# Performance work log

Measured on AMD Instinct MI355X. Metric: run time of the kernel, lower is better.

The kernel has to match this reference:

```python
import jax, jax.numpy as jnp
import numpy as np

LAYERS, HIDDEN, FFN, HEADS = 4, 128, 256, 4
HEAD_D = HIDDEN // HEADS          # 32
V_HEAD = 2 * HEAD_D               # 64 (double_v_dim)
V_DIM = 2 * HIDDEN                # 256
SCALE_BASE = 512
EPS = 1e-5
GAMMAS = (1.0 - np.exp(np.linspace(np.log(1.0 / 32), np.log(1.0 / 512), HEADS))).astype(np.float32)


def _xpos(x, downscale):
    # x: (..., L, d) -- xpos rotary embedding with per-position decay scale
    L, d = x.shape[-2], x.shape[-1]
    half = d // 2
    base_scale = (jnp.arange(half, dtype=jnp.float32) + 0.4 * d) / (1.4 * d)   # (half,)
    power = jnp.arange(L, dtype=jnp.float32)[:, None] / SCALE_BASE
    sc = base_scale[None, :] ** power                                          # (L, half)
    inv_freq = 1.0 / (10000.0 ** (jnp.arange(half, dtype=jnp.float32) / half))
    ang = jnp.arange(L, dtype=jnp.float32)[:, None] * inv_freq[None, :]        # (L, half)
    sin, cos = jnp.sin(ang), jnp.cos(ang)
    if downscale:
        sc = 1.0 / sc
    sin_d = jnp.repeat(sin * sc, 2, axis=-1)   # duplicate_interleave -> (L, d)
    cos_d = jnp.repeat(cos * sc, 2, axis=-1)
    x1, x2 = x[..., ::2], x[..., 1::2]
    rot = jnp.stack((-x2, x1), axis=-1).reshape(x.shape)  # rotate_every_two
    return x * cos_d + rot * sin_d


def _layer_norm(x, w, b):
    mu = x.mean(-1, keepdims=True)
    var = x.var(-1, keepdims=True)
    return (x - mu) / jnp.sqrt(var + EPS) * w + b


def _msr(X, wq, wk, wv, wg, wo, gn_w, gn_b):
    # MultiScaleRetention, parallel form. X: (B, L, HIDDEN)
    B, L, _ = X.shape
    Q = _xpos(jnp.einsum('blh,nhd->bnld', X, wq), False)   # (B, heads, L, 32)
    K = _xpos(jnp.einsum('blh,nhd->bnld', X, wk), True)
    V = jnp.einsum('blh,nhv->bnlv', X, wv)                 # (B, heads, L, 64)
    n = jnp.arange(L)
    diff = n[:, None] - n[None, :]
    gam = jnp.asarray(GAMMAS)[:, None, None]
    D = jnp.where(diff >= 0, gam ** jnp.maximum(diff, 0).astype(jnp.float32), 0.0)  # (heads, L, L)
    scores = jnp.einsum('bnld,bnmd->bnlm', Q, K) * D[None]
    Y = jnp.einsum('bnlm,bnmv->bnlv', scores, V)
    Y = Y.transpose(0, 2, 1, 3).reshape(B, L, V_DIM)       # concat heads on feature dim
    # GroupNorm(heads, V_DIM) over the channel axis
    Yg = Y.reshape(B, L, HEADS, V_HEAD)
    mu = Yg.mean(-1, keepdims=True)
    var = Yg.var(-1, keepdims=True)
    Yn = ((Yg - mu) / jnp.sqrt(var + EPS)).reshape(B, L, V_DIM) * gn_w + gn_b
    G = X @ wg
    return (G * jax.nn.sigmoid(G) * Yn) @ wo               # swish gate, output proj


def _forward(x, rem_w1, rem_b1, rem_w2, rem_b2, rem_w3, rem_b3,
             wq, wk, wv, wg, wo, gn_w, gn_b,
             ln1_w, ln1_b, ln2_w, ln2_b,
             ffn_w1, ffn_b1, ffn_w2, ffn_b2,
             dec_w1, dec_b1, dec_w2, dec_b2):
    gelu = lambda t: jax.nn.gelu(t, approximate=False)
    # REM: 5 -> 32 -> 64 -> 128, GELU after each linear
    X = gelu(gelu(gelu(x @ rem_w1 + rem_b1) @ rem_w2 + rem_b2) @ rem_w3 + rem_b3)
    # RetNet: pre-LN retention + pre-LN FFN blocks with residuals
    for i in range(LAYERS):
        Y = _msr(_layer_norm(X, ln1_w[i], ln1_b[i]), wq[i], wk[i], wv[i],
                 wg[i], wo[i], gn_w[i], gn_b[i]) + X
        Z = _layer_norm(Y, ln2_w[i], ln2_b[i])
        X = gelu(Z @ ffn_w1[i] + ffn_b1[i]) @ ffn_w2[i] + ffn_b2[i] + Y
    # Decoder: 128 -> 64 -> 20, softmax over classes
    logits = gelu(X @ dec_w1 + dec_b1) @ dec_w2 + dec_b2
    return jax.nn.softmax(logits, axis=-1)


def setup_inputs() -> dict:
    key = jax.random.key(0)
    ks = jax.random.split(key, 16)
    rn = lambda k, shape, s=0.02: jax.random.normal(k, shape, dtype=jnp.float32) * s
    B, L = 64, 512
    return {
        'x': jax.random.normal(ks[0], (B, L, 5), dtype=jnp.float32),
        'rem_w1': rn(ks[1], (5, 32)), 'rem_b1': jnp.zeros((32,), jnp.float32),
        'rem_w2': rn(ks[2], (32, 64)), 'rem_b2': jnp.zeros((64,), jnp.float32),
        'rem_w3': rn(ks[3], (64, HIDDEN)), 'rem_b3': jnp.zeros((HIDDEN,), jnp.float32),
        'wq': rn(ks[4], (LAYERS, HEADS, HIDDEN, HEAD_D), 1.0 / HIDDEN),
        'wk': rn(ks[5], (LAYERS, HEADS, HIDDEN, HEAD_D), 1.0 / HIDDEN),
        'wv': rn(ks[6], (LAYERS, HEADS, HIDDEN, V_HEAD), 1.0 / HIDDEN),
        'wg': rn(ks[7], (LAYERS, HIDDEN, V_DIM), 1.0 / HIDDEN),
        'wo': rn(ks[8], (LAYERS, V_DIM, HIDDEN), 1.0 / HIDDEN),
        'gn_w': jnp.ones((LAYERS, V_DIM), jnp.float32),
        'gn_b': jnp.zeros((LAYERS, V_DIM), jnp.float32),
        'ln1_w': jnp.ones((LAYERS, HIDDEN), jnp.float32),
        'ln1_b': jnp.zeros((LAYERS, HIDDEN), jnp.float32),
        'ln2_w': jnp.ones((LAYERS, HIDDEN), jnp.float32),
        'ln2_b': jnp.zeros((LAYERS, HIDDEN), jnp.float32),
        'ffn_w1': rn(ks[9], (LAYERS, HIDDEN, FFN)),
        'ffn_b1': jnp.zeros((LAYERS, FFN), jnp.float32),
        'ffn_w2': rn(ks[10], (LAYERS, FFN, HIDDEN)),
        'ffn_b2': jnp.zeros((LAYERS, HIDDEN), jnp.float32),
        'dec_w1': rn(ks[11], (HIDDEN, 64)), 'dec_b1': jnp.zeros((64,), jnp.float32),
        'dec_w2': rn(ks[12], (64, 20)), 'dec_b2': jnp.zeros((20,), jnp.float32),
    }


def reference(x, rem_w1, rem_b1, rem_w2, rem_b2, rem_w3, rem_b3,
              wq, wk, wv, wg, wo, gn_w, gn_b,
              ln1_w, ln1_b, ln2_w, ln2_b,
              ffn_w1, ffn_b1, ffn_w2, ffn_b2,
              dec_w1, dec_b1, dec_w2, dec_b2):
    return _forward(x, rem_w1, rem_b1, rem_w2, rem_b2, rem_w3, rem_b3,
                    wq, wk, wv, wg, wo, gn_w, gn_b,
                    ln1_w, ln1_b, ln2_w, ln2_b,
                    ffn_w1, ffn_b1, ffn_w2, ffn_b2,
                    dec_w1, dec_b1, dec_w2, dec_b2)
```

## Files before the change

### kernel.cpp

```cpp
#include <hip/hip_runtime.h>
#include <math.h>
#include <cmath>

#define SEQ   512
#define NBATCH 64
#define BT    32768
#define HID   128
#define NHEAD 4
#define HD    32
#define VHD   64
#define VDIM  256
#define FFND  256

typedef __attribute__((ext_vector_type(8))) short bf16x8;
typedef __attribute__((ext_vector_type(4))) float f32x4;
typedef unsigned short u16;

__device__ __forceinline__ float gelu_f(float x){ return 0.5f*x*(1.f+erff(x*0.70710678118f)); }

__device__ __forceinline__ u16 f2bf(float f){
  union{float f; unsigned u;} v; v.f = f;
  unsigned r = v.u + 0x7FFF + ((v.u>>16)&1);
  return (u16)(r>>16);
}
__device__ __forceinline__ float bf2f(u16 u){
  union{unsigned u; float f;} v; v.u = ((unsigned)u)<<16; return v.f;
}

__device__ __forceinline__ void gload16(const void* g, void* l){
  __builtin_amdgcn_global_load_lds(
      (const __attribute__((address_space(1))) unsigned*)g,
      (__attribute__((address_space(3))) unsigned*)l, 16, 0, 0);
}

#define STAGE_TILE(dst, base, strideU16, colOffU16, wid_, srow_, phys16l_)      \
  do{                                                                           \
    _Pragma("unroll")                                                           \
    for(int it_=0; it_<8; it_++){                                               \
      int blk_ = (wid_)*8 + it_;                                                \
      int row_ = blk_*4 + (srow_);                                              \
      int log16_ = (phys16l_) ^ (row_&15);                                      \
      gload16((base) + (size_t)row_*(strideU16) + (colOffU16) + log16_*8,       \
              &(dst)[blk_*512]);                                                \
    }                                                                           \
  }while(0)

__global__ __launch_bounds__(256) void wconv_kernel(
    const float* __restrict__ wq, const float* __restrict__ wk,
    const float* __restrict__ wv, const float* __restrict__ wg,
    const float* __restrict__ wo, const float* __restrict__ f1,
    const float* __restrict__ f2, const float* __restrict__ dw1,
    const float* __restrict__ w2e, const float* __restrict__ w3e,
    u16* __restrict__ Wt)
{
  int idx = blockIdx.x*256 + threadIdx.x;
  if(idx >= 786432){
    int q = idx - 786432;
    if(q < 8192){ int col=q>>7, h=q&127; Wt[idx]=f2bf(dw1[h*64+col]); }
    else if(q < 10240){ int p=q-8192; int row=p>>5, col=p&31; Wt[idx]=f2bf(w2e[col*64+row]); }
    else { int p=q-10240; int row=p>>6, col=p&63; Wt[idx]=f2bf(w3e[col*128+row]); }
    return;
  }
  int layer = idx / 196608;
  int r = idx - layer*196608;
  u16* W = Wt + (size_t)layer*196608;
  const float* wq_l = wq + (size_t)layer*16384;
  const float* wk_l = wk + (size_t)layer*16384;
  const float* wv_l = wv + (size_t)layer*32768;
  const float* wg_l = wg + (size_t)layer*32768;
  const float* wo_l = wo + (size_t)layer*32768;
  const float* f1_l = f1 + (size_t)layer*32768;
  const float* f2_l = f2 + (size_t)layer*32768;
  float v;
  if(r < 98304){
    int col = r>>7, h = r&127;
    if(col<128){ int n=col>>5, d=col&31; v = wq_l[(n*128+h)*32+d]; }
    else if(col<256){ int c=col-128, n=c>>5, d=c&31; v = wk_l[(n*128+h)*32+d]; }
    else if(col<512){ int c=col-256, n=c>>6, j=c&63; v = wv_l[(n*128+h)*64+j]; }
    else { int p=col-512; v = wg_l[h*256+p]; }
    W[r] = f2bf(v);
  } else if(r < 131072){
    int q = r-98304; int col=q>>8, k=q&255;
    W[r] = f2bf(wo_l[k*128+col]);
  } else if(r < 163840){
    int q = r-131072; int col=q>>7, h=q&127;
    W[r] = f2bf(f1_l[h*256+col]);
  } else {
    int q = r-163840; int col=q>>8, k=q&255;
    W[r] = f2bf(f2_l[k*128+col]);
  }
}

__global__ __launch_bounds__(256) void embed_kernel(
    const float* __restrict__ x,
    const float* __restrict__ w1, const float* __restrict__ b1,
    const float* __restrict__ b2, const float* __restrict__ b3,
    const u16* __restrict__ W23t,
    const float* __restrict__ lnw, const float* __restrict__ lnb,
    float* __restrict__ X, u16* __restrict__ xn)
{
  __shared__ float sx[64][6];
  __shared__ float sw1[160], sb1[32], sb2[64], sb3[128];
  __shared__ u16 big[18944];
  int t=threadIdx.x, lane=t&63, wid=t>>6, mrow=lane&15, quad=lane>>4, r0=wid*16;
  int tok0=blockIdx.x*64;

  for(int i=t;i<320;i+=256) sx[i/5][i%5]=x[(size_t)tok0*5+i];
  for(int i=t;i<160;i+=256) sw1[i]=w1[i];
  if(t<32) sb1[t]=b1[t];
  if(t<64) sb2[t]=b2[t];
  if(t<128) sb3[t]=b3[t];
  for(int c=t;c<256;c+=256){ int row=c>>2, c8=(c&3)*8;
    *(uint4*)&big[2560+row*40+c8]=*(const uint4*)&W23t[row*32+c8]; }
  for(int c=t;c<1024;c+=256){ int row=c>>3, c8=(c&7)*8;
    *(uint4*)&big[9728+row*72+c8]=*(const uint4*)&W23t[2048+row*64+c8]; }
  __syncthreads();

  for(int task=t; task<2048; task+=256){
    int tok=task>>5, j=task&31;
    float a=sb1[j];
    #pragma unroll
    for(int i=0;i<5;i++) a+=sx[tok][i]*sw1[i*32+j];
    big[tok*40+j]=f2bf(gelu_f(a));
  }
  __syncthreads();

  f32x4 h2[4];
  #pragma unroll
  for(int cc=0;cc<4;cc++) h2[cc]=(f32x4){0.f,0.f,0.f,0.f};
  {
    bf16x8 a=*(const bf16x8*)&big[(r0+mrow)*40+quad*8];
    #pragma unroll
    for(int cc=0;cc<4;cc++){
      bf16x8 b=*(const bf16x8*)&big[2560+(cc*16+mrow)*40+quad*8];
      h2[cc]=__builtin_amdgcn_mfma_f32_16x16x32_bf16(a,b,h2[cc],0,0,0);
    }
  }
  #pragma unroll
  for(int cc=0;cc<4;cc++){
    float bs=sb2[cc*16+mrow];
    #pragma unroll
    for(int reg=0;reg<4;reg++)
      big[5120+(r0+quad*4+reg)*72+cc*16+mrow]=f2bf(gelu_f(h2[cc][reg]+bs));
  }
  __syncthreads();

  f32x4 xac[8];
  #pragma unroll
  for(int cc=0;cc<8;cc++) xac[cc]=(f32x4){0.f,0.f,0.f,0.f};
  #pragma unroll
  for(int ks=0;ks<2;ks++){
    bf16x8 a=*(const bf16x8*)&big[5120+(r0+mrow)*72+ks*32+quad*8];
    #pragma unroll
    for(int cc=0;cc<8;cc++){
      bf16x8 b=*(const bf16x8*)&big[9728+(cc*16+mrow)*72+ks*32+quad*8];
      xac[cc]=__builtin_amdgcn_mfma_f32_16x16x32_bf16(a,b,xac[cc],0,0,0);
    }
  }
  __syncthreads();

  #pragma unroll
  for(int reg=0;reg<4;reg++){
    int rowl=r0+quad*4+reg, rowg=tok0+rowl;
    float xv[8], s=0.f, sq=0.f;
    #pragma unroll
    for(int cc=0;cc<8;cc++){
      float v=gelu_f(xac[cc][reg]+sb3[cc*16+mrow]);
      xv[cc]=v; s+=v; sq+=v*v;
    }
    #pragma unroll
    for(int m=1;m<16;m<<=1){ s+=__shfl_xor(s,m); sq+=__shfl_xor(sq,m); }
    float mu=s*(1.f/128.f);
    float var=sq*(1.f/128.f)-mu*mu;
    float rstd=rsqrtf(var+1e-5f);
    #pragma unroll
    for(int cc=0;cc<8;cc++){
      int col=cc*16+mrow;
      X[(size_t)rowg*128+col]=xv[cc];
      big[rowl*136+col]=f2bf((xv[cc]-mu)*rstd*lnw[col]+lnb[col]);
    }
  }
  __syncthreads();
  for(int th=t; th<1024; th+=256){
    int row=th>>4, seg=th&15;
    *(uint4*)&xn[(size_t)(tok0+row)*128+seg*8]=*(const uint4*)&big[row*136+seg*8];
  }
}

__device__ __forceinline__ void qkvg_epilogue(
    int nc, f32x4 acc[2][4], u16* stg,
    int t, int mrow, int quad, int r0q, int c0q, int b, int l0, int tok0,
    u16* __restrict__ Q, u16* __restrict__ K,
    u16* __restrict__ Vt, u16* __restrict__ G)
{
  if(nc < 2){
    bool isK = (nc==1);
    float sgn = isK ? -1.f : 1.f;
    #pragma unroll
    for(int cc=0;cc<4;cc++){
      int colc = c0q + cc*16 + mrow;
      int i = (colc&31)>>1;
      float log2bs = log2f(((float)i + 12.8f)*(1.f/44.8f));
      float invf   = exp2f(-(float)i * (13.28771238f/16.f));
      float rstep  = exp2f(sgn*log2bs*(1.f/512.f));
      float c1 = cosf(invf), s1 = sinf(invf);
      #pragma unroll
      for(int rr=0;rr<2;rr++){
        int rowl0 = r0q + rr*16 + quad*4;
        float lb = (float)(l0 + rowl0);
        float sc = exp2f(sgn*log2bs*lb*(1.f/512.f));
        float ang = lb*invf;
        float u = cosf(ang)*sc, v = sinf(ang)*sc;
        #pragma unroll
        for(int reg=0;reg<4;reg++){
          int rowl = rowl0 + reg;
          float val = acc[rr][cc][reg];
          float partner = __shfl_xor(val, 1);
          float o = (colc&1) ? (val*u + partner*v) : (val*u - partner*v);
          stg[rowl*136 + colc] = f2bf(o);
          float un = (u*c1 - v*s1)*rstep;
          float vn = (u*s1 + v*c1)*rstep;
          u = un; v = vn;
        }
      }
    }
    __syncthreads();
    u16* O = isK ? K : Q;
    for(int th=t; th<1024; th+=256){
      int row=th>>4, n=(th>>2)&3, seg=th&3;
      *(uint4*)&O[(((size_t)(b*4+n)*512) + (l0+row))*32 + seg*8]
        = *(const uint4*)&stg[row*136 + n*32 + seg*8];
    }
  } else if(nc < 4){
    #pragma unroll
    for(int cc=0;cc<4;cc++){
      int colc = c0q + cc*16 + mrow;
      #pragma unroll
      for(int rr=0;rr<2;rr++){
        #pragma unroll
        for(int reg=0;reg<4;reg++){
          int rowl = r0q + rr*16 + quad*4 + reg;
          stg[colc*72 + rowl] = f2bf(acc[rr][cc][reg]);
        }
      }
    }
    __syncthreads();
    int jbase = (nc-2)*128;
    for(int th=t; th<1024; th+=256){
      int row=th>>3, seg=th&7;
      int jg = jbase + row; int n = jg>>6, j = jg&63;
      *(uint4*)&Vt[(((size_t)(b*4+n)*64) + j)*512 + l0 + seg*8]
        = *(const uint4*)&stg[row*72 + seg*8];
    }
  } else {
    #pragma unroll
    for(int cc=0;cc<4;cc++){
      int colc = c0q + cc*16 + mrow;
      #pragma unroll
      for(int rr=0;rr<2;rr++){
        #pragma unroll
        for(int reg=0;reg<4;reg++){
          int rowl = r0q + rr*16 + quad*4 + reg;
          stg[rowl*136 + colc] = f2bf(acc[rr][cc][reg]);
        }
      }
    }
    __syncthreads();
    int gc0 = (nc-4)*128;
    for(int th=t; th<1024; th+=256){
      int row=th>>4, seg=th&15;
      *(uint4*)&G[((size_t)(tok0+row))*256 + gc0 + seg*8]
        = *(const uint4*)&stg[row*136 + seg*8];
    }
  }
}

__global__ __launch_bounds__(256) void qkvg_kernel(
    const u16* __restrict__ A, const u16* __restrict__ Wt,
    u16* __restrict__ Q, u16* __restrict__ K,
    u16* __restrict__ Vt, u16* __restrict__ G)
{
  __shared__ u16 sW[128*128];
  u16* stg = sW;
  int t = threadIdx.x, lane = t&63, wid = t>>6;
  int mrow = lane&15, quad = lane>>4;
  int srow = lane>>4, phys16l = lane&15;
  int r0q = (wid>>1)*32, c0q = (wid&1)*64;
  int tok0 = blockIdx.x*64;
  int b = tok0>>9, l0 = tok0&511;

  bf16x8 a0f[4], a1f[4];
  #pragma unroll
  for(int ks=0; ks<4; ks++){
    a0f[ks] = *(const bf16x8*)&A[(size_t)(tok0+r0q+mrow)*128 + ks*32+quad*8];
    a1f[ks] = *(const bf16x8*)&A[(size_t)(tok0+r0q+16+mrow)*128 + ks*32+quad*8];
  }

  for(int ch=0; ch<3; ch++){
    int nc = blockIdx.y*3 + ch;
    if(ch) __syncthreads();
    STAGE_TILE(sW, Wt + (size_t)nc*16384, 128, 0, wid, srow, phys16l);
    __syncthreads();

    f32x4 acc[2][4];
    #pragma unroll
    for(int rr=0;rr<2;rr++)
      #pragma unroll
      for(int cc=0;cc<4;cc++) acc[rr][cc] = (f32x4){0.f,0.f,0.f,0.f};
    #pragma unroll
    for(int ks=0; ks<4; ks++){
      #pragma unroll
      for(int cc=0; cc<4; cc++){
        bf16x8 bb = *(const bf16x8*)&sW[(c0q+cc*16+mrow)*128 + (((ks*4+quad)^mrow)<<3)];
        acc[0][cc] = __builtin_amdgcn_mfma_f32_16x16x32_bf16(a0f[ks],bb,acc[0][cc],0,0,0);
        acc[1][cc] = __builtin_amdgcn_mfma_f32_16x16x32_bf16(a1f[ks],bb,acc[1][cc],0,0,0);
      }
    }
    __syncthreads();
    qkvg_epilogue(nc, acc, stg, t, mrow, quad, r0q, c0q, b, l0, tok0, Q, K, Vt, G);
  }
}

__global__ __launch_bounds__(256) void mlpq_kernel(
    const u16* __restrict__ Gated, const u16* __restrict__ Wo,
    const u16* __restrict__ W1t, const float* __restrict__ b1,
    const u16* __restrict__ W2t, const float* __restrict__ b2,
    const float* __restrict__ Xin,
    const float* __restrict__ ln2w, const float* __restrict__ ln2b,
    const float* __restrict__ ln1w, const float* __restrict__ ln1b,
    float* __restrict__ Xout,
    const u16* __restrict__ Wq,
    u16* __restrict__ Q, u16* __restrict__ K,
    u16* __restrict__ Vt, u16* __restrict__ G)
{
  __shared__ u16 sW[128*128];
  __shared__ u16 sT[64*136];
  int t=threadIdx.x, lane=t&63, wid=t>>6, mrow=lane&15, quad=lane>>4, r0=wid*16;
  int tok0=blockIdx.x*64;
  int srow = lane>>4, phys16l = lane&15;

  bf16x8 gfrag[8];
  #pragma unroll
  for(int ks=0;ks<8;ks++)
    gfrag[ks]=*(const bf16x8*)&Gated[(size_t)(tok0+r0+mrow)*256 + ks*32+quad*8];

  f32x4 yac[8];
  #pragma unroll
  for(int ch=0;ch<8;ch++) yac[ch]=(f32x4){0.f,0.f,0.f,0.f};
  STAGE_TILE(sW, Wo, 256, 0, wid, srow, phys16l);
  __syncthreads();
  #pragma unroll
  for(int kh=0; kh<2; kh++){
    #pragma unroll
    for(int ch=0;ch<8;ch++){
      #pragma unroll
      for(int ks=0;ks<4;ks++){
        bf16x8 b=*(const bf16x8*)&sW[(ch*16+mrow)*128 + (((ks*4+quad)^mrow)<<3)];
        yac[ch]=__builtin_amdgcn_mfma_f32_16x16x32_bf16(gfrag[kh*4+ks],b,yac[ch],0,0,0);
      }
    }
    if(kh==0){
      __syncthreads();
      STAGE_TILE(sW, Wo, 256, 128, wid, srow, phys16l);
      __syncthreads();
    }
  }

  float yv[8][4];
  #pragma unroll
  for(int reg=0;reg<4;reg++){
    int rowl=r0+quad*4+reg, rowg=tok0+rowl;
    float s=0.f, sq=0.f;
    #pragma unroll
    for(int ch=0;ch<8;ch++){
      float v=yac[ch][reg]+Xin[(size_t)rowg*128+ch*16+mrow];
      yv[ch][reg]=v; s+=v; sq+=v*v;
    }
    #pragma unroll
    for(int m=1;m<16;m<<=1){ s+=__shfl_xor(s,m); sq+=__shfl_xor(sq,m); }
    float mu=s*(1.f/128.f);
    float var=sq*(1.f/128.f)-mu*mu;
    float rstd=rsqrtf(var+1e-5f);
    #pragma unroll
    for(int ch=0;ch<8;ch++){
      int col=ch*16+mrow;
      sT[rowl*136+col]=f2bf((yv[ch][reg]-mu)*rstd*ln2w[col]+ln2b[col]);
    }
  }
  bf16x8 az[4];
  #pragma unroll
  for(int ks=0;ks<4;ks++) az[ks]=*(const bf16x8*)&sT[(r0+mrow)*136+ks*32+quad*8];
  __syncthreads();

  bf16x8 hfrag[8];
  #pragma unroll
  for(int nh=0; nh<2; nh++){
    STAGE_TILE(sW, W1t + (size_t)nh*16384, 128, 0, wid, srow, phys16l);
    __syncthreads();
    f32x4 hac[8];
    #pragma unroll
    for(int ch=0;ch<8;ch++) hac[ch]=(f32x4){0.f,0.f,0.f,0.f};
    #pragma unroll
    for(int ch=0;ch<8;ch++){
      #pragma unroll
      for(int ks=0;ks<4;ks++){
        bf16x8 b=*(const bf16x8*)&sW[(ch*16+mrow)*128 + (((ks*4+quad)^mrow)<<3)];
        hac[ch]=__builtin_amdgcn_mfma_f32_16x16x32_bf16(az[ks],b,hac[ch],0,0,0);
      }
    }
    #pragma unroll
    for(int ch=0;ch<8;ch++){
      float bs=b1[nh*128+ch*16+mrow];
      #pragma unroll
      for(int reg=0;reg<4;reg++)
        sT[(r0+quad*4+reg)*136 + ch*16+mrow]=f2bf(gelu_f(hac[ch][reg]+bs));
    }
    #pragma unroll
    for(int ks=0;ks<4;ks++) hfrag[nh*4+ks]=*(const bf16x8*)&sT[(r0+mrow)*136+ks*32+quad*8];
    __syncthreads();
  }

  f32x4 xac[8];
  #pragma unroll
  for(int ch=0;ch<8;ch++) xac[ch]=(f32x4){0.f,0.f,0.f,0.f};
  STAGE_TILE(sW, W2t, 256, 0, wid, srow, phys16l);
  __syncthreads();
  #pragma unroll
  for(int kh=0; kh<2; kh++){
    #pragma unroll
    for(int ch=0;ch<8;ch++){
      #pragma unroll
      for(int ks=0;ks<4;ks++){
        bf16x8 b=*(const bf16x8*)&sW[(ch*16+mrow)*128 + (((ks*4+quad)^mrow)<<3)];
        xac[ch]=__builtin_amdgcn_mfma_f32_16x16x32_bf16(hfrag[kh*4+ks],b,xac[ch],0,0,0);
      }
    }
    __syncthreads();
    if(kh==0){
      STAGE_TILE(sW, W2t, 256, 128, wid, srow, phys16l);
      __syncthreads();
    }
  }

  float* fst = (float*)sW;
  #pragma unroll
  for(int reg=0;reg<4;reg++){
    int rowl=r0+quad*4+reg;
    float xv[8], s=0.f, sq=0.f;
    #pragma unroll
    for(int ch=0;ch<8;ch++){
      float v=xac[ch][reg]+b2[ch*16+mrow]+yv[ch][reg];
      xv[ch]=v; s+=v; sq+=v*v;
    }
    #pragma unroll
    for(int m=1;m<16;m<<=1){ s+=__shfl_xor(s,m); sq+=__shfl_xor(sq,m); }
    float mu=s*(1.f/128.f);
    float var=sq*(1.f/128.f)-mu*mu;
    float rstd=rsqrtf(var+1e-5f);
    #pragma unroll
    for(int ch=0;ch<8;ch++){
      int col=ch*16+mrow;
      fst[rowl*128+col]=xv[ch];
      sT[rowl*136+col]=f2bf((xv[ch]-mu)*rstd*ln1w[col]+ln1b[col]);
    }
  }
  __syncthreads();
  for(int th=t; th<2048; th+=256){
    int row=th>>5, c4=(th&31)*4;
    *(float4*)&Xout[(size_t)(tok0+row)*128+c4]=*(const float4*)&fst[row*128+c4];
  }

  if(!Wq) return;

  int r0q = (wid>>1)*32, c0q = (wid&1)*64;
  int b = tok0>>9, l0 = tok0&511;
  bf16x8 a0f[4], a1f[4];
  #pragma unroll
  for(int ks=0; ks<4; ks++){
    a0f[ks] = *(const bf16x8*)&sT[(r0q+mrow)*136 + ks*32+quad*8];
    a1f[ks] = *(const bf16x8*)&sT[(r0q+16+mrow)*136 + ks*32+quad*8];
  }
  __syncthreads();

  for(int nc=0; nc<6; nc++){
    if(nc) __syncthreads();
    STAGE_TILE(sW, Wq + (size_t)nc*16384, 128, 0, wid, srow, phys16l);
    __syncthreads();

    f32x4 acc[2][4];
    #pragma unroll
    for(int rr=0;rr<2;rr++)
      #pragma unroll
      for(int cc=0;cc<4;cc++) acc[rr][cc] = (f32x4){0.f,0.f,0.f,0.f};
    #pragma unroll
    for(int ks=0; ks<4; ks++){
      #pragma unroll
      for(int cc=0; cc<4; cc++){
        bf16x8 bb = *(const bf16x8*)&sW[(c0q+cc*16+mrow)*128 + (((ks*4+quad)^mrow)<<3)];
        acc[0][cc] = __builtin_amdgcn_mfma_f32_16x16x32_bf16(a0f[ks],bb,acc[0][cc],0,0,0);
        acc[1][cc] = __builtin_amdgcn_mfma_f32_16x16x32_bf16(a1f[ks],bb,acc[1][cc],0,0,0);
      }
    }
    __syncthreads();
    qkvg_epilogue(nc, acc, sW, t, mrow, quad, r0q, c0q, b, l0, tok0, Q, K, Vt, G);
  }
}

__global__ __launch_bounds__(256) void retmfma_kernel(
    const u16* __restrict__ Q, const u16* __restrict__ K,
    const u16* __restrict__ Vt, const u16* __restrict__ G,
    const float* __restrict__ gnw, const float* __restrict__ gnb,
    u16* __restrict__ Gated, float4 log2g)
{
  int idx = blockIdx.x;
  int bn = ((idx>>6)<<3) | (idx&7);
  int lt = (idx>>3)&7;
  int n = bn & 3, b = bn >> 2;
  float lg2g = (n==0)?log2g.x:(n==1)?log2g.y:(n==2)?log2g.z:log2g.w;
  __shared__ u16 sK[64][40];
  __shared__ u16 sVt[64][72];
  __shared__ u16 sS[64][72];
  int t = threadIdx.x, lane = t&63, wid = t>>6;
  int mrow = lane&15, quad = lane>>4;
  int r0 = wid*16;

  bf16x8 qa = *(const bf16x8*)&Q[((size_t)bn*512 + lt*64 + r0+mrow)*32 + quad*8];

  f32x4 oacc[4];
  #pragma unroll
  for(int cc=0;cc<4;cc++) oacc[cc] = (f32x4){0.f,0.f,0.f,0.f};
  float gp1 = exp2f(lg2g), gp2 = gp1*gp1, gp3 = gp2*gp1;
  float gpow[4] = {1.f, gp1, gp2, gp3};
  float gw[4], gb[4];
  #pragma unroll
  for(int cc=0;cc<4;cc++){ gw[cc]=gnw[n*64+cc*16+mrow]; gb[cc]=gnb[n*64+cc*16+mrow]; }
  int rowl0 = lt*64 + r0 + quad*4;

  for(int mt=0; mt<=lt; mt++){
    if(mt) __syncthreads();
    {
      int row = t>>2, c8 = (t&3)*8;
      *(uint4*)&sK[row][c8] = *(const uint4*)&K[((size_t)bn*512 + mt*64 + row)*32 + c8];
      int vrow = t>>3, vc8 = (t&7)*8;
      *(uint4*)&sVt[vrow][vc8]    = *(const uint4*)&Vt[((size_t)bn*64 + vrow)*512    + mt*64 + vc8];
      *(uint4*)&sVt[vrow+32][vc8] = *(const uint4*)&Vt[((size_t)bn*64 + vrow+32)*512 + mt*64 + vc8];
    }
    __syncthreads();
    f32x4 sacc[4];
    #pragma unroll
    for(int cc=0;cc<4;cc++){
      bf16x8 bb = *(const bf16x8*)&sK[cc*16+mrow][quad*8];
      sacc[cc] = __builtin_amdgcn_mfma_f32_16x16x32_bf16(qa,bb,(f32x4){0.f,0.f,0.f,0.f},0,0,0);
    }
    #pragma unroll
    for(int cc=0;cc<4;cc++){
      int colm = mt*64 + cc*16 + mrow;
      int d0 = rowl0 - colm;
      float w0 = exp2f(lg2g*(float)d0);
      #pragma unroll
      for(int reg=0;reg<4;reg++){
        float w = (d0+reg>=0) ? w0*gpow[reg] : 0.f;
        sS[r0+quad*4+reg][cc*16+mrow] = f2bf(sacc[cc][reg]*w);
      }
    }
    __syncthreads();
    #pragma unroll
    for(int ks=0;ks<2;ks++){
      bf16x8 a = *(const bf16x8*)&sS[r0+mrow][ks*32+quad*8];
      #pragma unroll
      for(int cc=0;cc<4;cc++){
        bf16x8 bb = *(const bf16x8*)&sVt[cc*16+mrow][ks*32+quad*8];
        oacc[cc] = __builtin_amdgcn_mfma_f32_16x16x32_bf16(a,bb,oacc[cc],0,0,0);
      }
    }
  }

  __syncthreads();
  #pragma unroll
  for(int reg=0;reg<4;reg++){
    float s=0.f, sq=0.f;
    #pragma unroll
    for(int cc=0;cc<4;cc++){ float v=oacc[cc][reg]; s+=v; sq+=v*v; }
    #pragma unroll
    for(int m=1;m<16;m<<=1){ s+=__shfl_xor(s,m); sq+=__shfl_xor(sq,m); }
    float mu = s*(1.f/64.f);
    float var = sq*(1.f/64.f) - mu*mu;
    float rn = rsqrtf(var + 1e-5f);
    int rowl = r0 + quad*4 + reg;
    int l = lt*64 + rowl;
    size_t gbase = ((size_t)(b*512 + l))*256 + n*64;
    #pragma unroll
    for(int cc=0;cc<4;cc++){
      float gg = bf2f(G[gbase + cc*16+mrow]);
      float gate = gg/(1.f+expf(-gg));
      sS[rowl][cc*16+mrow] = f2bf(gate*((oacc[cc][reg]-mu)*rn*gw[cc] + gb[cc]));
    }
  }
  __syncthreads();
  for(int th=t; th<512; th+=256){
    int row=th>>3, seg=th&7;
    *(uint4*)&Gated[((size_t)(b*512 + lt*64 + row))*256 + n*64 + seg*8]
      = *(const uint4*)&sS[row][seg*8];
  }
}

__global__ __launch_bounds__(256) void dec_kernel(
    const float* __restrict__ X, const u16* __restrict__ W1t,
    const float* __restrict__ b1, const float* __restrict__ w2,
    const float* __restrict__ b2, float* __restrict__ out)
{
  __shared__ u16 sA[64][136];
  __shared__ u16 sW[64][136];
  __shared__ float sH[64][68];
  __shared__ float sL[64*20];
  __shared__ float sw2[64*20];
  __shared__ float sb2[20];
  int t = threadIdx.x, lane = t&63, wid = t>>6;
  int mrow = lane&15, quad = lane>>4;
  int tok0 = blockIdx.x*64;

  for(int th=t; th<2048; th+=256){
    int row=th>>5, c4=(th&31)*4;
    float4 v = *(const float4*)&X[(size_t)(tok0+row)*128 + c4];
    ushort4 p; p.x=f2bf(v.x); p.y=f2bf(v.y); p.z=f2bf(v.z); p.w=f2bf(v.w);
    *(ushort4*)&sA[row][c4] = p;
  }
  for(int th=t; th<1024; th+=256){
    int row=th>>4, c8=(th&15)*8;
    *(uint4*)&sW[row][c8] = *(const uint4*)&W1t[(size_t)row*128 + c8];
  }
  for(int i=t;i<1280;i+=256) sw2[i]=w2[i];
  if(t<20) sb2[t]=b2[t];
  __syncthreads();

  int r0 = wid*16;
  f32x4 acc[4];
  #pragma unroll
  for(int cc=0;cc<4;cc++) acc[cc] = (f32x4){0.f,0.f,0.f,0.f};
  #pragma unroll
  for(int ks=0; ks<4; ks++){
    int koff = ks*32 + quad*8;
    bf16x8 a = *(const bf16x8*)&sA[r0+mrow][koff];
    #pragma unroll
    for(int cc=0; cc<4; cc++){
      bf16x8 b = *(const bf16x8*)&sW[cc*16+mrow][koff];
      acc[cc] = __builtin_amdgcn_mfma_f32_16x16x32_bf16(a,b,acc[cc],0,0,0);
    }
  }
  #pragma unroll
  for(int cc=0;cc<4;cc++){
    int col = cc*16 + mrow;
    float bb = b1[col];
    #pragma unroll
    for(int reg=0;reg<4;reg++){
      sH[r0 + quad*4 + reg][col] = gelu_f(acc[cc][reg] + bb);
    }
  }
  __syncthreads();

  for(int task=t; task<1280; task+=256){
    int tk = task/20, o = task - tk*20;
    float a = sb2[o];
    for(int k=0;k<64;k++) a += sH[tk][k]*sw2[k*20+o];
    sL[tk*20+o] = a;
  }
  __syncthreads();
  if(t < 64){
    float mx = -1e30f;
    #pragma unroll
    for(int o=0;o<20;o++) mx = fmaxf(mx, sL[t*20+o]);
    float sum = 0.f;
    float e[20];
    #pragma unroll
    for(int o=0;o<20;o++){ e[o]=expf(sL[t*20+o]-mx); sum += e[o]; }
    float inv = 1.f/sum;
    #pragma unroll
    for(int o=0;o<20;o++) sL[t*20+o] = e[o]*inv;
  }
  __syncthreads();
  for(int th=t; th<1280; th+=256){
    out[(size_t)tok0*20 + th] = sL[th];
  }
}

extern "C" void kernel_launch(void* const* d_in, const int* in_sizes, int n_in,
                              void* d_out, int out_size, void* d_ws, size_t ws_size,
                              hipStream_t stream) {
  (void)in_sizes; (void)n_in; (void)out_size; (void)ws_size;
  const float* x      = (const float*)d_in[0];
  const float* rem_w1 = (const float*)d_in[1];
  const float* rem_b1 = (const float*)d_in[2];
  const float* rem_w2 = (const float*)d_in[3];
  const float* rem_b2 = (const float*)d_in[4];
  const float* rem_w3 = (const float*)d_in[5];
  const float* rem_b3 = (const float*)d_in[6];
  const float* wq     = (const float*)d_in[7];
  const float* wk     = (const float*)d_in[8];
  const float* wv     = (const float*)d_in[9];
  const float* wg     = (const float*)d_in[10];
  const float* wo     = (const float*)d_in[11];
  const float* gn_w   = (const float*)d_in[12];
  const float* gn_b   = (const float*)d_in[13];
  const float* ln1_w  = (const float*)d_in[14];
  const float* ln1_b  = (const float*)d_in[15];
  const float* ln2_w  = (const float*)d_in[16];
  const float* ln2_b  = (const float*)d_in[17];
  const float* ffn_w1 = (const float*)d_in[18];
  const float* ffn_b1 = (const float*)d_in[19];
  const float* ffn_w2 = (const float*)d_in[20];
  const float* ffn_b2 = (const float*)d_in[21];
  const float* dec_w1 = (const float*)d_in[22];
  const float* dec_b1 = (const float*)d_in[23];
  const float* dec_w2 = (const float*)d_in[24];
  const float* dec_b2 = (const float*)d_in[25];
  float* outp = (float*)d_out;

  const size_t S128 = (size_t)BT*128;
  const size_t S256 = (size_t)BT*256;
  float* ws = (float*)d_ws;
  float* Xb = ws;
  u16*  Qb16    = (u16*)(Xb + S128);
  u16*  Kb16    = Qb16 + (size_t)BT*32;
  u16*  Vt16    = Kb16 + (size_t)BT*32;
  u16*  XnBf    = Vt16 + (size_t)BT*64;
  u16*  GBf     = XnBf + S128;
  u16*  GatedBf = GBf + S256;
  u16*  WtBf    = GatedBf + S256;

  double lgA = log(1.0/32.0), lgB = log(1.0/512.0);
  float4 l2g;
  {
    double g0 = 1.0 - exp(lgA + 0.0*(lgB-lgA)/3.0);
    double g1 = 1.0 - exp(lgA + 1.0*(lgB-lgA)/3.0);
    double g2 = 1.0 - exp(lgA + 2.0*(lgB-lgA)/3.0);
    double g3 = 1.0 - exp(lgA + 3.0*(lgB-lgA)/3.0);
    l2g.x = (float)(log(g0)/log(2.0));
    l2g.y = (float)(log(g1)/log(2.0));
    l2g.z = (float)(log(g2)/log(2.0));
    l2g.w = (float)(log(g3)/log(2.0));
  }

  wconv_kernel<<<3144, 256, 0, stream>>>(wq, wk, wv, wg, wo, ffn_w1, ffn_w2, dec_w1,
                                         rem_w2, rem_w3, WtBf);
  embed_kernel<<<BT/64, 256, 0, stream>>>(x, rem_w1, rem_b1, rem_b2, rem_b3,
                                          WtBf+794624, ln1_w, ln1_b, Xb, XnBf);
  qkvg_kernel<<<dim3(BT/64,2), 256, 0, stream>>>(XnBf, WtBf, Qb16, Kb16, Vt16, GBf);

  for(int li=0; li<4; li++){
    u16* Wt_l = WtBf + (size_t)li*196608;
    const float* gnw_l = gn_w + (size_t)li*VDIM;
    const float* gnb_l = gn_b + (size_t)li*VDIM;
    const float* l2w = ln2_w + (size_t)li*HID, *l2b = ln2_b + (size_t)li*HID;
    const float* f1b = ffn_b1 + (size_t)li*FFND;
    const float* f2b = ffn_b2 + (size_t)li*HID;
    int nli = (li+1)&3;
    const float* n1w = ln1_w + (size_t)nli*HID, *n1b = ln1_b + (size_t)nli*HID;
    const u16* Wq_next = (li<3) ? (WtBf + (size_t)(li+1)*196608) : nullptr;

    retmfma_kernel<<<2048, 256, 0, stream>>>(Qb16, Kb16, Vt16, GBf, gnw_l, gnb_l, GatedBf, l2g);
    mlpq_kernel<<<BT/64, 256, 0, stream>>>(
        GatedBf, Wt_l+98304, Wt_l+131072, f1b, Wt_l+163840, f2b,
        Xb, l2w, l2b, n1w, n1b, Xb,
        Wq_next, Qb16, Kb16, Vt16, GBf);
  }

  dec_kernel<<<BT/64, 256, 0, stream>>>(Xb, WtBf+786432, dec_b1, dec_w2, dec_b2, outp);
}
```

Measured before the change: 452.6 us.

## Split mlpq work across eight waves with column halves and shared LayerNorm reduction

The fused MLP/QKVG kernel now launches 512 threads instead of 256. Each row group of 16 tokens is split across two waves that each own half of the output columns. LayerNorm statistics are combined across the two waves through a small shared-memory reduction, and weight staging, epilogues and QKVG projection are adapted to the narrower per-wave tiles. The aim is more waves per block to hide latency and cut per-thread register pressure, at the cost of extra barriers and shared-memory traffic.

```diff
diff --git a/kernel.cpp b/kernel.cpp
--- a/kernel.cpp
+++ b/kernel.cpp
@@ -33,17 +33,20 @@
       (__attribute__((address_space(3))) unsigned*)l, 16, 0, 0);
 }
 
-#define STAGE_TILE(dst, base, strideU16, colOffU16, wid_, srow_, phys16l_)      \
+#define STAGE_TILE_N(dst, base, strideU16, colOffU16, wid_, srow_, phys16l_, NIT) \
   do{                                                                           \
     _Pragma("unroll")                                                           \
-    for(int it_=0; it_<8; it_++){                                               \
-      int blk_ = (wid_)*8 + it_;                                                \
+    for(int it_=0; it_<NIT; it_++){                                             \
+      int blk_ = (wid_)*NIT + it_;                                              \
       int row_ = blk_*4 + (srow_);                                              \
       int log16_ = (phys16l_) ^ (row_&15);                                      \
       gload16((base) + (size_t)row_*(strideU16) + (colOffU16) + log16_*8,       \
               &(dst)[blk_*512]);                                                \
     }                                                                           \
   }while(0)
+
+#define STAGE_TILE(dst, base, strideU16, colOffU16, wid_, srow_, phys16l_) \
+  STAGE_TILE_N(dst, base, strideU16, colOffU16, wid_, srow_, phys16l_, 8)
 
 __global__ __launch_bounds__(256) void wconv_kernel(
     const float* __restrict__ wq, const float* __restrict__ wk,
@@ -275,6 +278,85 @@
   }
 }
 
+__device__ __forceinline__ void qkvg_epi8(
+    int nc, f32x4 acc[4], u16* stg,
+    int t, int mrow, int quad, int r0, int c0, int b, int l0, int tok0,
+    u16* __restrict__ Q, u16* __restrict__ K,
+    u16* __restrict__ Vt, u16* __restrict__ G)
+{
+  if(nc < 2){
+    bool isK = (nc==1);
+    float sgn = isK ? -1.f : 1.f;
+    #pragma unroll
+    for(int cc=0;cc<4;cc++){
+      int colc = c0 + cc*16 + mrow;
+      int i = (colc&31)>>1;
+      float log2bs = log2f(((float)i + 12.8f)*(1.f/44.8f));
+      float invf   = exp2f(-(float)i * (13.28771238f/16.f));
+      float rstep  = exp2f(sgn*log2bs*(1.f/512.f));
+      float c1 = cosf(invf), s1 = sinf(invf);
+      int rowl0 = r0 + quad*4;
+      float lb = (float)(l0 + rowl0);
+      float sc = exp2f(sgn*log2bs*lb*(1.f/512.f));
+      float ang = lb*invf;
+      float u = cosf(ang)*sc, v = sinf(ang)*sc;
+      #pragma unroll
+      for(int reg=0;reg<4;reg++){
+        int rowl = rowl0 + reg;
+        float val = acc[cc][reg];
+        float partner = __shfl_xor(val, 1);
+        float o = (colc&1) ? (val*u + partner*v) : (val*u - partner*v);
+        stg[rowl*136 + colc] = f2bf(o);
+        float un = (u*c1 - v*s1)*rstep;
+        float vn = (u*s1 + v*c1)*rstep;
+        u = un; v = vn;
+      }
+    }
+    __syncthreads();
+    u16* O = isK ? K : Q;
+    for(int th=t; th<1024; th+=512){
+      int row=th>>4, n=(th>>2)&3, seg=th&3;
+      *(uint4*)&O[(((size_t)(b*4+n)*512) + (l0+row))*32 + seg*8]
+        = *(const uint4*)&stg[row*136 + n*32 + seg*8];
+    }
+  } else if(nc < 4){
+    #pragma unroll
+    for(int cc=0;cc<4;cc++){
+      int colc = c0 + cc*16 + mrow;
+      #pragma unroll
+      for(int reg=0;reg<4;reg++){
+        int rowl = r0 + quad*4 + reg;
+        stg[colc*72 + rowl] = f2bf(acc[cc][reg]);
+      }
+    }
+    __syncthreads();
+    int jbase = (nc-2)*128;
+    for(int th=t; th<1024; th+=512){
+      int row=th>>3, seg=th&7;
+      int jg = jbase + row; int n = jg>>6, j = jg&63;
+      *(uint4*)&Vt[(((size_t)(b*4+n)*64) + j)*512 + l0 + seg*8]
+        = *(const uint4*)&stg[row*72 + seg*8];
+    }
+  } else {
+    #pragma unroll
+    for(int cc=0;cc<4;cc++){
+      int colc = c0 + cc*16 + mrow;
+      #pragma unroll
+      for(int reg=0;reg<4;reg++){
+        int rowl = r0 + quad*4 + reg;
+        stg[rowl*136 + colc] = f2bf(acc[cc][reg]);
+      }
+    }
+    __syncthreads();
+    int gc0 = (nc-4)*128;
+    for(int th=t; th<1024; th+=512){
+      int row=th>>4, seg=th&15;
+      *(uint4*)&G[((size_t)(tok0+row))*256 + gc0 + seg*8]
+        = *(const uint4*)&stg[row*136 + seg*8];
+    }
+  }
+}
+
 __global__ __launch_bounds__(256) void qkvg_kernel(
     const u16* __restrict__ A, const u16* __restrict__ Wt,
     u16* __restrict__ Q, u16* __restrict__ K,
@@ -321,7 +403,7 @@
   }
 }
 
-__global__ __launch_bounds__(256) void mlpq_kernel(
+__global__ __launch_bounds__(512, 4) void mlpq_kernel(
     const u16* __restrict__ Gated, const u16* __restrict__ Wo,
     const u16* __restrict__ W1t, const float* __restrict__ b1,
     const u16* __restrict__ W2t, const float* __restrict__ b2,
@@ -335,7 +417,10 @@
 {
   __shared__ u16 sW[128*128];
   __shared__ u16 sT[64*136];
-  int t=threadIdx.x, lane=t&63, wid=t>>6, mrow=lane&15, quad=lane>>4, r0=wid*16;
+  __shared__ float sRed[64][2][2];
+  int t=threadIdx.x, lane=t&63, wid=t>>6, mrow=lane&15, quad=lane>>4;
+  int rg=wid>>1, half=wid&1;
+  int r0=rg*16, c0=half*64;
   int tok0=blockIdx.x*64;
   int srow = lane>>4, phys16l = lane&15;
 
@@ -344,165 +429,177 @@
   for(int ks=0;ks<8;ks++)
     gfrag[ks]=*(const bf16x8*)&Gated[(size_t)(tok0+r0+mrow)*256 + ks*32+quad*8];
 
-  f32x4 yac[8];
-  #pragma unroll
-  for(int ch=0;ch<8;ch++) yac[ch]=(f32x4){0.f,0.f,0.f,0.f};
-  STAGE_TILE(sW, Wo, 256, 0, wid, srow, phys16l);
+  f32x4 yac[4];
+  #pragma unroll
+  for(int cc=0;cc<4;cc++) yac[cc]=(f32x4){0.f,0.f,0.f,0.f};
+  STAGE_TILE_N(sW, Wo, 256, 0, wid, srow, phys16l, 4);
   __syncthreads();
   #pragma unroll
   for(int kh=0; kh<2; kh++){
     #pragma unroll
-    for(int ch=0;ch<8;ch++){
+    for(int cc=0;cc<4;cc++){
       #pragma unroll
       for(int ks=0;ks<4;ks++){
-        bf16x8 b=*(const bf16x8*)&sW[(ch*16+mrow)*128 + (((ks*4+quad)^mrow)<<3)];
-        yac[ch]=__builtin_amdgcn_mfma_f32_16x16x32_bf16(gfrag[kh*4+ks],b,yac[ch],0,0,0);
+        bf16x8 b=*(const bf16x8*)&sW[(c0+cc*16+mrow)*128 + (((ks*4+quad)^mrow)<<3)];
+        yac[cc]=__builtin_amdgcn_mfma_f32_16x16x32_bf16(gfrag[kh*4+ks],b,yac[cc],0,0,0);
       }
     }
     if(kh==0){
       __syncthreads();
-      STAGE_TILE(sW, Wo, 256, 128, wid, srow, phys16l);
+      STAGE_TILE_N(sW, Wo, 256, 128, wid, srow, phys16l, 4);
       __syncthreads();
     }
   }
 
-  float yv[8][4];
+  float yv[4][4];
   #pragma unroll
   for(int reg=0;reg<4;reg++){
     int rowl=r0+quad*4+reg, rowg=tok0+rowl;
     float s=0.f, sq=0.f;
     #pragma unroll
-    for(int ch=0;ch<8;ch++){
-      float v=yac[ch][reg]+Xin[(size_t)rowg*128+ch*16+mrow];
-      yv[ch][reg]=v; s+=v; sq+=v*v;
+    for(int cc=0;cc<4;cc++){
+      float v=yac[cc][reg]+Xin[(size_t)rowg*128+c0+cc*16+mrow];
+      yv[cc][reg]=v; s+=v; sq+=v*v;
     }
     #pragma unroll
     for(int m=1;m<16;m<<=1){ s+=__shfl_xor(s,m); sq+=__shfl_xor(sq,m); }
+    if(mrow==0){ sRed[rowl][half][0]=s; sRed[rowl][half][1]=sq; }
+  }
+  __syncthreads();
+  #pragma unroll
+  for(int reg=0;reg<4;reg++){
+    int rowl=r0+quad*4+reg;
+    float s =sRed[rowl][0][0]+sRed[rowl][1][0];
+    float sq=sRed[rowl][0][1]+sRed[rowl][1][1];
     float mu=s*(1.f/128.f);
     float var=sq*(1.f/128.f)-mu*mu;
     float rstd=rsqrtf(var+1e-5f);
     #pragma unroll
-    for(int ch=0;ch<8;ch++){
-      int col=ch*16+mrow;
-      sT[rowl*136+col]=f2bf((yv[ch][reg]-mu)*rstd*ln2w[col]+ln2b[col]);
-    }
-  }
+    for(int cc=0;cc<4;cc++){
+      int col=c0+cc*16+mrow;
+      sT[rowl*136+col]=f2bf((yv[cc][reg]-mu)*rstd*ln2w[col]+ln2b[col]);
+    }
+  }
+  __syncthreads();
   bf16x8 az[4];
   #pragma unroll
   for(int ks=0;ks<4;ks++) az[ks]=*(const bf16x8*)&sT[(r0+mrow)*136+ks*32+quad*8];
-  __syncthreads();
 
   bf16x8 hfrag[8];
   #pragma unroll
   for(int nh=0; nh<2; nh++){
-    STAGE_TILE(sW, W1t + (size_t)nh*16384, 128, 0, wid, srow, phys16l);
-    __syncthreads();
-    f32x4 hac[8];
-    #pragma unroll
-    for(int ch=0;ch<8;ch++) hac[ch]=(f32x4){0.f,0.f,0.f,0.f};
-    #pragma unroll
-    for(int ch=0;ch<8;ch++){
+    STAGE_TILE_N(sW, W1t + (size_t)nh*16384, 128, 0, wid, srow, phys16l, 4);
+    __syncthreads();
+    f32x4 hac[4];
+    #pragma unroll
+    for(int cc=0;cc<4;cc++) hac[cc]=(f32x4){0.f,0.f,0.f,0.f};
+    #pragma unroll
+    for(int cc=0;cc<4;cc++){
       #pragma unroll
       for(int ks=0;ks<4;ks++){
-        bf16x8 b=*(const bf16x8*)&sW[(ch*16+mrow)*128 + (((ks*4+quad)^mrow)<<3)];
-        hac[ch]=__builtin_amdgcn_mfma_f32_16x16x32_bf16(az[ks],b,hac[ch],0,0,0);
-      }
-    }
-    #pragma unroll
-    for(int ch=0;ch<8;ch++){
-      float bs=b1[nh*128+ch*16+mrow];
+        bf16x8 b=*(const bf16x8*)&sW[(c0+cc*16+mrow)*128 + (((ks*4+quad)^mrow)<<3)];
+        hac[cc]=__builtin_amdgcn_mfma_f32_16x16x32_bf16(az[ks],b,hac[cc],0,0,0);
+      }
+    }
+    __syncthreads();
+    #pragma unroll
+    for(int cc=0;cc<4;cc++){
+      float bs=b1[nh*128+c0+cc*16+mrow];
       #pragma unroll
       for(int reg=0;reg<4;reg++)
-        sT[(r0+quad*4+reg)*136 + ch*16+mrow]=f2bf(gelu_f(hac[ch][reg]+bs));
-    }
+        sT[(r0+quad*4+reg)*136 + c0+cc*16+mrow]=f2bf(gelu_f(hac[cc][reg]+bs));
+    }
+    __syncthreads();
     #pragma unroll
     for(int ks=0;ks<4;ks++) hfrag[nh*4+ks]=*(const bf16x8*)&sT[(r0+mrow)*136+ks*32+quad*8];
-    __syncthreads();
-  }
-
-  f32x4 xac[8];
-  #pragma unroll
-  for(int ch=0;ch<8;ch++) xac[ch]=(f32x4){0.f,0.f,0.f,0.f};
-  STAGE_TILE(sW, W2t, 256, 0, wid, srow, phys16l);
+  }
+
+  f32x4 xac[4];
+  #pragma unroll
+  for(int cc=0;cc<4;cc++) xac[cc]=(f32x4){0.f,0.f,0.f,0.f};
+  STAGE_TILE_N(sW, W2t, 256, 0, wid, srow, phys16l, 4);
   __syncthreads();
   #pragma unroll
   for(int kh=0; kh<2; kh++){
     #pragma unroll
-    for(int ch=0;ch<8;ch++){
+    for(int cc=0;cc<4;cc++){
       #pragma unroll
       for(int ks=0;ks<4;ks++){
-        bf16x8 b=*(const bf16x8*)&sW[(ch*16+mrow)*128 + (((ks*4+quad)^mrow)<<3)];
-        xac[ch]=__builtin_amdgcn_mfma_f32_16x16x32_bf16(hfrag[kh*4+ks],b,xac[ch],0,0,0);
+        bf16x8 b=*(const bf16x8*)&sW[(c0+cc*16+mrow)*128 + (((ks*4+quad)^mrow)<<3)];
+        xac[cc]=__builtin_amdgcn_mfma_f32_16x16x32_bf16(hfrag[kh*4+ks],b,xac[cc],0,0,0);
       }
     }
     __syncthreads();
     if(kh==0){
-      STAGE_TILE(sW, W2t, 256, 128, wid, srow, phys16l);
+      STAGE_TILE_N(sW, W2t, 256, 128, wid, srow, phys16l, 4);
       __syncthreads();
     }
   }
 
   float* fst = (float*)sW;
+  float xv[4][4];
   #pragma unroll
   for(int reg=0;reg<4;reg++){
     int rowl=r0+quad*4+reg;
-    float xv[8], s=0.f, sq=0.f;
-    #pragma unroll
-    for(int ch=0;ch<8;ch++){
-      float v=xac[ch][reg]+b2[ch*16+mrow]+yv[ch][reg];
-      xv[ch]=v; s+=v; sq+=v*v;
+    float s=0.f, sq=0.f;
+    #pragma unroll
+    for(int cc=0;cc<4;cc++){
+      float v=xac[cc][reg]+b2[c0+cc*16+mrow]+yv[cc][reg];
+      xv[cc][reg]=v; s+=v; sq+=v*v;
     }
     #pragma unroll
     for(int m=1;m<16;m<<=1){ s+=__shfl_xor(s,m); sq+=__shfl_xor(sq,m); }
+    if(mrow==0){ sRed[rowl][half][0]=s; sRed[rowl][half][1]=sq; }
+  }
+  __syncthreads();
+  #pragma unroll
+  for(int reg=0;reg<4;reg++){
+    int rowl=r0+quad*4+reg;
+    float s =sRed[rowl][0][0]+sRed[rowl][1][0];
+    float sq=sRed[rowl][0][1]+sRed[rowl][1][1];
     float mu=s*(1.f/128.f);
     float var=sq*(1.f/128.f)-mu*mu;
     float rstd=rsqrtf(var+1e-5f);
     #pragma unroll
-    for(int ch=0;ch<8;ch++){
-      int col=ch*16+mrow;
-      fst[rowl*128+col]=xv[ch];
-      sT[rowl*136+col]=f2bf((xv[ch]-mu)*rstd*ln1w[col]+ln1b[col]);
-    }
-  }
-  __syncthreads();
-  for(int th=t; th<2048; th+=256){
+    for(int cc=0;cc<4;cc++){
+      int col=c0+cc*16+mrow;
+      fst[rowl*128+col]=xv[cc][reg];
+      sT[rowl*136+col]=f2bf((xv[cc][reg]-mu)*rstd*ln1w[col]+ln1b[col]);
+    }
+  }
+  __syncthreads();
+  for(int th=t; th<2048; th+=512){
     int row=th>>5, c4=(th&31)*4;
     *(float4*)&Xout[(size_t)(tok0+row)*128+c4]=*(const float4*)&fst[row*128+c4];
   }
 
   if(!Wq) return;
 
-  int r0q = (wid>>1)*32, c0q = (wid&1)*64;
   int b = tok0>>9, l0 = tok0&511;
-  bf16x8 a0f[4], a1f[4];
-  #pragma unroll
-  for(int ks=0; ks<4; ks++){
-    a0f[ks] = *(const bf16x8*)&sT[(r0q+mrow)*136 + ks*32+quad*8];
-    a1f[ks] = *(const bf16x8*)&sT[(r0q+16+mrow)*136 + ks*32+quad*8];
-  }
+  bf16x8 aq[4];
+  #pragma unroll
+  for(int ks=0; ks<4; ks++)
+    aq[ks] = *(const bf16x8*)&sT[(r0+mrow)*136 + ks*32+quad*8];
   __syncthreads();
 
   for(int nc=0; nc<6; nc++){
     if(nc) __syncthreads();
-    STAGE_TILE(sW, Wq + (size_t)nc*16384, 128, 0, wid, srow, phys16l);
-    __syncthreads();
-
-    f32x4 acc[2][4];
-    #pragma unroll
-    for(int rr=0;rr<2;rr++)
-      #pragma unroll
-      for(int cc=0;cc<4;cc++) acc[rr][cc] = (f32x4){0.f,0.f,0.f,0.f};
+    STAGE_TILE_N(sW, Wq + (size_t)nc*16384, 128, 0, wid, srow, phys16l, 4);
+    __syncthreads();
+
+    f32x4 acc[4];
+    #pragma unroll
+    for(int cc=0;cc<4;cc++) acc[cc] = (f32x4){0.f,0.f,0.f,0.f};
     #pragma unroll
     for(int ks=0; ks<4; ks++){
       #pragma unroll
       for(int cc=0; cc<4; cc++){
-        bf16x8 bb = *(const bf16x8*)&sW[(c0q+cc*16+mrow)*128 + (((ks*4+quad)^mrow)<<3)];
-        acc[0][cc] = __builtin_amdgcn_mfma_f32_16x16x32_bf16(a0f[ks],bb,acc[0][cc],0,0,0);
-        acc[1][cc] = __builtin_amdgcn_mfma_f32_16x16x32_bf16(a1f[ks],bb,acc[1][cc],0,0,0);
-      }
-    }
-    __syncthreads();
-    qkvg_epilogue(nc, acc, sW, t, mrow, quad, r0q, c0q, b, l0, tok0, Q, K, Vt, G);
+        bf16x8 bb = *(const bf16x8*)&sW[(c0+cc*16+mrow)*128 + (((ks*4+quad)^mrow)<<3)];
+        acc[cc] = __builtin_amdgcn_mfma_f32_16x16x32_bf16(aq[ks],bb,acc[cc],0,0,0);
+      }
+    }
+    __syncthreads();
+    qkvg_epi8(nc, acc, sW, t, mrow, quad, r0, c0, b, l0, tok0, Q, K, Vt, G);
   }
 }
 
@@ -758,7 +855,7 @@
     const u16* Wq_next = (li<3) ? (WtBf + (size_t)(li+1)*196608) : nullptr;
 
     retmfma_kernel<<<2048, 256, 0, stream>>>(Qb16, Kb16, Vt16, GBf, gnw_l, gnb_l, GatedBf, l2g);
-    mlpq_kernel<<<BT/64, 256, 0, stream>>>(
+    mlpq_kernel<<<BT/64, 512, 0, stream>>>(
         GatedBf, Wt_l+98304, Wt_l+131072, f1b, Wt_l+163840, f2b,
         Xb, l2w, l2b, n1w, n1b, Xb,
         Wq_next, Qb16, Kb16, Vt16, GBf);
```

Measured after the change: 454.7 us. Within noise of the previous version (+0.5%).
